# Kernel optimization log

Hardware: AMD Instinct MI355X
Metric: run time of the kernel (lower is better)

Reference implementation:

```python
import jax, jax.numpy as jnp
import numpy as np

BLOCK = 8           # block_size
FREQ_REMOVE = 2     # freq_remove_num


def _ceil16(n: int) -> int:
    # replicate DCT.padding: four rounds of ceil-div-2, then *16
    for _ in range(4):
        n = (n + 1) // 2
    return 16 * n


def _dct_mat(N: int) -> jnp.ndarray:
    # orthonormal DCT-II matrix D s.t. (D @ v) == scipy.fftpack.dct(v, norm='ortho')
    n = jnp.arange(N, dtype=jnp.float32)
    k = n[:, None]
    D = jnp.cos(jnp.pi * (2.0 * n[None, :] + 1.0) * k / (2.0 * N))
    scale = jnp.where(jnp.arange(N) == 0, jnp.sqrt(1.0 / N), jnp.sqrt(2.0 / N)).astype(jnp.float32)
    return D * scale[:, None]


def setup_inputs() -> dict:
    key = jax.random.key(0)
    x = jax.random.uniform(key, (1, 4096, 4096), dtype=jnp.float32)  # image in [0,1)
    return {"x": x}


def reference(x) -> jnp.ndarray:
    _, h, w = x.shape
    H, W = _ceil16(h), _ceil16(w)
    h1 = (H - h) // 2
    w1 = (W - w) // 2
    x = jnp.pad(x, ((0, 0), (h1, H - h - h1), (w1, W - w - w1)))
    # (x*255).byte(): truncation; inputs in [0,1) -> floor, no uint8 wrap
    x = jnp.floor(x * 255.0)
    Hb, Wb = H // BLOCK, W // BLOCK
    # [1,H,W] -> [Hb, Wb, b, b] (drop leading singleton like iterating .numpy())
    blk = x.reshape(Hb, BLOCK, Wb, BLOCK).transpose(0, 2, 1, 3)
    # Faithful to source: dct along axis=1 (Wb block-index axis) then axis=2 (block row axis)
    Dw = _dct_mat(Wb)      # [Wb, Wb]
    Db = _dct_mat(BLOCK)   # [b, b]
    y = jnp.einsum('kw,hwij->hkij', Dw, blk)   # DCT over block-column index
    y = jnp.einsum('mi,hkij->hkmj', Db, y)     # DCT over intra-block rows
    # retain_high_freq: zero first FREQ_REMOVE rows and cols of each bxb block
    mask = jnp.ones((BLOCK, BLOCK), y.dtype).at[:FREQ_REMOVE, :].set(0.0).at[:, :FREQ_REMOVE].set(0.0)
    y = y * mask  # broadcast over [Hb, Wb, b, b]
    # permute back and flatten to [1, H, W]
    out = y.transpose(0, 2, 1, 3).reshape(1, H, W)
    return out
```

## Files before the change

### kernel.cpp

```cpp
#include <hip/hip_runtime.h>
#include <math.h>

#define ZSLAB 98304
#define DSLAB 16384
#define SBUF  13312
#define OB_PITCH 392

typedef __attribute__((ext_vector_type(8))) __bf16 bf16x8;
typedef __attribute__((ext_vector_type(4))) float  f32x4;

__device__ __forceinline__ unsigned short f2bf(float f) {
  union { float f; unsigned u; } v; v.f = f;
  unsigned r = v.u + 0x7fffu + ((v.u >> 16) & 1u);
  return (unsigned short)(r >> 16);
}
__device__ __forceinline__ float bf2f_lo(unsigned u) {
  union { unsigned u; float f; } v; v.u = u << 16; return v.f;
}
__device__ __forceinline__ float bf2f_hi(unsigned u) {
  union { unsigned u; float f; } v; v.u = u & 0xffff0000u; return v.f;
}

__device__ const float DBC[8][8] = {
  { 0.35355339f,  0.35355339f,  0.35355339f,  0.35355339f,  0.35355339f,  0.35355339f,  0.35355339f,  0.35355339f},
  { 0.49039264f,  0.41573481f,  0.27778512f,  0.09754516f, -0.09754516f, -0.27778512f, -0.41573481f, -0.49039264f},
  { 0.46193977f,  0.19134172f, -0.19134172f, -0.46193977f, -0.46193977f, -0.19134172f,  0.19134172f,  0.46193977f},
  { 0.41573481f, -0.09754516f, -0.49039264f, -0.27778512f,  0.27778512f,  0.49039264f,  0.09754516f, -0.41573481f},
  { 0.35355339f, -0.35355339f, -0.35355339f,  0.35355339f,  0.35355339f, -0.35355339f, -0.35355339f,  0.35355339f},
  { 0.27778512f, -0.49039264f,  0.09754516f,  0.41573481f, -0.41573481f, -0.09754516f,  0.49039264f, -0.27778512f},
  { 0.19134172f, -0.46193977f,  0.46193977f, -0.19134172f, -0.19134172f,  0.46193977f, -0.46193977f,  0.19134172f},
  { 0.09754516f, -0.27778512f,  0.41573481f, -0.49039264f,  0.49039264f, -0.41573481f,  0.27778512f, -0.09754516f}
};

__global__ __launch_bounds__(256) void pack_all(const float* __restrict__ x,
                                                unsigned short* __restrict__ zc,
                                                unsigned short* __restrict__ dwf) {
  const int h = blockIdx.x, t = threadIdx.x;

  {
    const int idx = (blockIdx.y * 512 + blockIdx.x) * 256 + t;
    const int k = idx >> 9, w = idx & 511;
    const int n = (k * (2 * w + 1)) & 2047;
    const float c = __cosf((float)n * 0.0030679615757712823f);
    const float scale = (k == 0) ? 0.04419417382415922f : 0.0625f;
    const int kko = w >> 5, g = (w >> 3) & 3, e = w & 7, s = (k >> 1) & 3;
    dwf[(size_t)kko * DSLAB + k * 32 + ((g ^ s) << 3) + e] = f2bf(c * scale);
  }

  const int c0 = blockIdx.y * 2048 + t * 8;
  const float* xb = x + (size_t)(h * 8) * 4096 + c0;
  float q[8][8];
#pragma unroll
  for (int i = 0; i < 8; ++i) {
    float4 a = *reinterpret_cast<const float4*>(xb + (size_t)i * 4096);
    float4 b = *reinterpret_cast<const float4*>(xb + (size_t)i * 4096 + 4);
    q[i][0] = floorf(a.x * 255.0f); q[i][1] = floorf(a.y * 255.0f);
    q[i][2] = floorf(a.z * 255.0f); q[i][3] = floorf(a.w * 255.0f);
    q[i][4] = floorf(b.x * 255.0f); q[i][5] = floorf(b.y * 255.0f);
    q[i][6] = floorf(b.z * 255.0f); q[i][7] = floorf(b.w * 255.0f);
  }
  const int w0 = c0 >> 3;
  const int kko = w0 >> 5, g = (w0 >> 3) & 3, e = w0 & 7;
#pragma unroll
  for (int m = 2; m < 8; ++m) {
    const int row = h * 6 + (m - 2);
    const int s = (row >> 1) & 3;
    const size_t base = (size_t)row * 32 + ((g ^ s) << 3) + e;
#pragma unroll
    for (int j = 2; j < 8; ++j) {
      float v = 0.0f;
#pragma unroll
      for (int i = 0; i < 8; ++i) v = fmaf(DBC[m][i], q[i][j], v);
      zc[(size_t)((j - 2) * 16 + kko) * ZSLAB + base] = f2bf(v);
    }
  }
}

__device__ __forceinline__ void gload16(const unsigned short* g, unsigned short* l) {
  __builtin_amdgcn_global_load_lds(
      (__attribute__((address_space(1))) void*)(g),
      (__attribute__((address_space(3))) void*)(l),
      16, 0, 0);
}

__global__ __launch_bounds__(768, 3) void fused_dct(const unsigned short* __restrict__ zc,
                                                    const unsigned short* __restrict__ dwf,
                                                    float* __restrict__ out) {
  const int bid = blockIdx.x;
  const int mt  = bid & 63;
  const int np  = bid >> 6;

  __shared__ __align__(16) unsigned char SM[106496];
  unsigned short* SMu  = (unsigned short*)SM;
  unsigned short* Obuf = (unsigned short*)SM;

  const int tid  = threadIdx.x;
  const int lane = tid & 63;
  const int wv   = tid >> 6;
  const int j2   = wv >> 1;
  const int nh   = wv & 1;
  const int l15  = lane & 15;
  const int hi   = lane >> 4;

  const unsigned short *sA0, *sA1, *sB0, *sB1, *sB2, *sB3;
  int dA0, dA1, dB0, dB1, dB2, dB3;
  {
    const int f0 = tid, f1 = 576 + tid;
    sA0 = zc + (size_t)(f0 / 192) * 16 * ZSLAB + mt * 1536 + (f0 % 192) * 8;
    sA1 = zc + (size_t)(f1 / 192) * 16 * ZSLAB + mt * 1536 + (f1 % 192) * 8;
    dA0 = f0 * 8; dA1 = f1 * 8;
    const int bt = tid - 576;
    const int g0 = bt, g1 = 128 + bt, g2 = 256 + bt, g3 = 384 + bt;
    sB0 = dwf + (np * 2 + 0) * 2048 + (g0 & 255) * 8;
    sB1 = dwf + (np * 2 + 0) * 2048 + (g1 & 255) * 8;
    sB2 = dwf + (np * 2 + 1) * 2048 + (g2 & 255) * 8;
    sB3 = dwf + (np * 2 + 1) * 2048 + (g3 & 255) * 8;
    dB0 = 9216 + g0 * 8; dB1 = 9216 + g1 * 8; dB2 = 9216 + g2 * 8; dB3 = 9216 + g3 * 8;
  }

#define STAGE(buf, kko)                                                       \
  do {                                                                        \
    unsigned short* L_ = SMu + (buf) * SBUF;                                  \
    if (tid < 576) {                                                          \
      gload16(sA0 + (size_t)(kko) * ZSLAB, L_ + dA0);                         \
      gload16(sA1 + (size_t)(kko) * ZSLAB, L_ + dA1);                         \
    } else if (tid < 704) {                                                   \
      gload16(sB0 + (size_t)(kko) * DSLAB, L_ + dB0);                         \
      gload16(sB1 + (size_t)(kko) * DSLAB, L_ + dB1);                         \
      gload16(sB2 + (size_t)(kko) * DSLAB, L_ + dB2);                         \
      gload16(sB3 + (size_t)(kko) * DSLAB, L_ + dB3);                         \
    }                                                                         \
  } while (0)

  float* const zbase = out + (size_t)(mt * 64) * 4096 + np * 1024;
#define WAITW(na, nb, t)                                                      \
  do {                                                                        \
    if (wv < 9) {                                                             \
      asm volatile("s_waitcnt vmcnt(" #na ")" ::: "memory");                  \
      __builtin_amdgcn_sched_barrier(0);                                      \
    } else if (wv < 11) {                                                     \
      asm volatile("s_waitcnt vmcnt(" #nb ")" ::: "memory");                  \
      __builtin_amdgcn_sched_barrier(0);                                      \
    } else {                                                                  \
      _Pragma("unroll")                                                       \
      for (int q_ = 0; q_ < 4; ++q_) {                                        \
        const int e_ = (t) * 4 + q_;                                          \
        const int r16_ = e_ >> 2;                                             \
        float* p_ = zbase + (size_t)((r16_ >> 1) * 8 + (r16_ & 1)) * 4096 +   \
                    (e_ & 3) * 256 + lane * 4;                                \
        *reinterpret_cast<f32x4*>(p_) = (f32x4){0.f, 0.f, 0.f, 0.f};          \
      }                                                                       \
    }                                                                         \
  } while (0)

  int aoff[3], boffA[2], boffB[2];
#pragma unroll
  for (int mf = 0; mf < 3; ++mf) {
    const int r_ = mf * 16 + l15;
    aoff[mf] = j2 * 1536 + r_ * 32 + ((hi ^ ((r_ >> 1) & 3)) << 3);
  }
#pragma unroll
  for (int nf = 0; nf < 2; ++nf) {
    const int r_ = nh * 32 + nf * 16 + l15;
    const int sw = r_ * 32 + ((hi ^ ((r_ >> 1) & 3)) << 3);
    boffA[nf] = 9216 + sw;
    boffB[nf] = 11264 + sw;
  }

  f32x4 accA[3][2] = {}, accB[3][2] = {};

  STAGE(0, 0); STAGE(1, 1); STAGE(2, 2); STAGE(3, 3);
#pragma unroll
  for (int t = 0; t < 16; ++t) {
    if (t <= 12)      WAITW(6, 12, t);
    else if (t == 13) WAITW(4, 8, t);
    else if (t == 14) WAITW(2, 4, t);
    else              WAITW(0, 0, t);
    __builtin_amdgcn_s_barrier();
    {
      const unsigned short* Bb = SMu + (t & 3) * SBUF;
      bf16x8 afr[3], bfa[2], bfb[2];
#pragma unroll
      for (int mf = 0; mf < 3; ++mf)
        afr[mf] = *reinterpret_cast<const bf16x8*>(Bb + aoff[mf]);
#pragma unroll
      for (int nf = 0; nf < 2; ++nf) {
        bfa[nf] = *reinterpret_cast<const bf16x8*>(Bb + boffA[nf]);
        bfb[nf] = *reinterpret_cast<const bf16x8*>(Bb + boffB[nf]);
      }
      __builtin_amdgcn_s_setprio(1);
#pragma unroll
      for (int mf = 0; mf < 3; ++mf) {
        accA[mf][0] = __builtin_amdgcn_mfma_f32_16x16x32_bf16(afr[mf], bfa[0], accA[mf][0], 0, 0, 0);
        accA[mf][1] = __builtin_amdgcn_mfma_f32_16x16x32_bf16(afr[mf], bfa[1], accA[mf][1], 0, 0, 0);
        accB[mf][0] = __builtin_amdgcn_mfma_f32_16x16x32_bf16(afr[mf], bfb[0], accB[mf][0], 0, 0, 0);
        accB[mf][1] = __builtin_amdgcn_mfma_f32_16x16x32_bf16(afr[mf], bfb[1], accB[mf][1], 0, 0, 0);
      }
      __builtin_amdgcn_s_setprio(0);
    }
    asm volatile("s_waitcnt lgkmcnt(0)" ::: "memory");
    __builtin_amdgcn_s_barrier();
    if (t <= 11) STAGE(t & 3, t + 4);
  }
#undef STAGE
#undef WAITW

  __syncthreads();

#pragma unroll
  for (int tt = 0; tt < 2; ++tt) {
#pragma unroll
    for (int mf = 0; mf < 3; ++mf)
#pragma unroll
      for (int nf = 0; nf < 2; ++nf)
#pragma unroll
        for (int p = 0; p < 4; ++p) {
          const float vv = tt ? accB[mf][nf][p] : accA[mf][nf][p];
          Obuf[(mf * 16 + hi * 4 + p) * OB_PITCH + (nh * 32 + nf * 16 + l15) * 6 + j2] =
              f2bf(vv);
        }
    asm volatile("s_waitcnt lgkmcnt(0)" ::: "memory");
    __builtin_amdgcn_s_barrier();

    float* outt = out + (size_t)(mt * 64) * 4096 + (np * 2 + tt) * 512;
    for (int v = tid; v < 6144; v += 768) {
      const int row48 = v >> 7;
      const int c4 = (v & 127) << 2;
      const int hg = row48 / 6, mm = row48 - hg * 6;
      const int row64 = hg * 8 + 2 + mm;
      const int kk = c4 >> 3, jb = c4 & 4;
      const unsigned short* Ob = Obuf + row48 * OB_PITCH + kk * 6;
      const unsigned ua = *(const unsigned*)(Ob + (jb >> 1));
      const unsigned ub = *(const unsigned*)(Ob + 4);
      f32x4 val;
      if (jb) {
        val[0] = bf2f_lo(ua); val[1] = bf2f_hi(ua);
        val[2] = bf2f_lo(ub); val[3] = bf2f_hi(ub);
      } else {
        val[0] = 0.f; val[1] = 0.f;
        val[2] = bf2f_lo(ua); val[3] = bf2f_hi(ua);
      }
      *reinterpret_cast<f32x4*>(outt + (size_t)row64 * 4096 + c4) = val;
    }
    if (tt == 0) {
      asm volatile("s_waitcnt lgkmcnt(0)" ::: "memory");
      __builtin_amdgcn_s_barrier();
    }
  }
}

extern "C" void kernel_launch(void* const* d_in, const int* in_sizes, int n_in,
                              void* d_out, int out_size, void* d_ws, size_t ws_size,
                              hipStream_t stream) {
  const float* x = (const float*)d_in[0];
  float* out = (float*)d_out;
  char* ws = (char*)d_ws;

  unsigned short* dwf = (unsigned short*)ws;
  unsigned short* zc  = (unsigned short*)(ws + 524288);

  pack_all<<<dim3(512, 2), 256, 0, stream>>>(x, zc, dwf);
  fused_dct<<<256, 768, 0, stream>>>(zc, dwf, out);
}
```

Before: 41.88 us.

## Double K-step per stage with two larger LDS buffers and single-pass epilogue

The K loop now processes two K sub-slices per pipeline stage (8 iterations instead of 16), using two double-sized LDS buffers instead of four smaller ones. Each stage issues twice as many global-to-LDS loads and twice as many zero-fill stores. The epilogue writes both output halves to LDS at once and stores them in one pass, which removes a barrier round. This cuts barriers and waitcnt stalls, but pipeline prefetch depth drops from 3 stages ahead to 1, which risks exposing load latency.

```diff
diff --git a/kernel.cpp b/kernel.cpp
--- a/kernel.cpp
+++ b/kernel.cpp
@@ -3,8 +3,8 @@
 
 #define ZSLAB 98304
 #define DSLAB 16384
-#define SBUF  13312
-#define OB_PITCH 392
+#define SBUF  26624
+#define OB_PITCH 776
 
 typedef __attribute__((ext_vector_type(8))) __bf16 bf16x8;
 typedef __attribute__((ext_vector_type(4))) float  f32x4;
@@ -102,33 +102,36 @@
   const int l15  = lane & 15;
   const int hi   = lane >> 4;
 
-  const unsigned short *sA0, *sA1, *sB0, *sB1, *sB2, *sB3;
-  int dA0, dA1, dB0, dB1, dB2, dB3;
-  {
-    const int f0 = tid, f1 = 576 + tid;
-    sA0 = zc + (size_t)(f0 / 192) * 16 * ZSLAB + mt * 1536 + (f0 % 192) * 8;
-    sA1 = zc + (size_t)(f1 / 192) * 16 * ZSLAB + mt * 1536 + (f1 % 192) * 8;
-    dA0 = f0 * 8; dA1 = f1 * 8;
-    const int bt = tid - 576;
-    const int g0 = bt, g1 = 128 + bt, g2 = 256 + bt, g3 = 384 + bt;
-    sB0 = dwf + (np * 2 + 0) * 2048 + (g0 & 255) * 8;
-    sB1 = dwf + (np * 2 + 0) * 2048 + (g1 & 255) * 8;
-    sB2 = dwf + (np * 2 + 1) * 2048 + (g2 & 255) * 8;
-    sB3 = dwf + (np * 2 + 1) * 2048 + (g3 & 255) * 8;
-    dB0 = 9216 + g0 * 8; dB1 = 9216 + g1 * 8; dB2 = 9216 + g2 * 8; dB3 = 9216 + g3 * 8;
-  }
-
-#define STAGE(buf, kko)                                                       \
+  const unsigned short *sA[4], *sB[8];
+  int dA[4], dB[8];
+  if (tid < 576) {
+#pragma unroll
+    for (int q = 0; q < 4; ++q) {
+      const int f = q * 576 + tid;
+      sA[q] = zc + (size_t)((f / 384) * 16 + (f % 384) / 192) * ZSLAB + mt * 1536 +
+              (f % 192) * 8;
+      dA[q] = f * 8;
+    }
+  } else if (tid < 704) {
+#pragma unroll
+    for (int q = 0; q < 8; ++q) {
+      const int g = q * 128 + (tid - 576);
+      sB[q] = dwf + (size_t)(g >> 9) * DSLAB + np * 4096 + (g & 511) * 8;
+      dB[q] = 18432 + g * 8;
+    }
+  }
+
+#define STAGE(buf, kk)                                                        \
   do {                                                                        \
     unsigned short* L_ = SMu + (buf) * SBUF;                                  \
     if (tid < 576) {                                                          \
-      gload16(sA0 + (size_t)(kko) * ZSLAB, L_ + dA0);                         \
-      gload16(sA1 + (size_t)(kko) * ZSLAB, L_ + dA1);                         \
+      _Pragma("unroll")                                                       \
+      for (int q_ = 0; q_ < 4; ++q_)                                          \
+        gload16(sA[q_] + (size_t)(2 * (kk)) * ZSLAB, L_ + dA[q_]);            \
     } else if (tid < 704) {                                                   \
-      gload16(sB0 + (size_t)(kko) * DSLAB, L_ + dB0);                         \
-      gload16(sB1 + (size_t)(kko) * DSLAB, L_ + dB1);                         \
-      gload16(sB2 + (size_t)(kko) * DSLAB, L_ + dB2);                         \
-      gload16(sB3 + (size_t)(kko) * DSLAB, L_ + dB3);                         \
+      _Pragma("unroll")                                                       \
+      for (int q_ = 0; q_ < 8; ++q_)                                          \
+        gload16(sB[q_] + (size_t)(2 * (kk)) * DSLAB, L_ + dB[q_]);            \
     }                                                                         \
   } while (0)
 
@@ -143,9 +146,9 @@
       __builtin_amdgcn_sched_barrier(0);                                      \
     } else {                                                                  \
       _Pragma("unroll")                                                       \
-      for (int q_ = 0; q_ < 4; ++q_) {                                        \
-        const int e_ = (t) * 4 + q_;                                          \
-        const int r16_ = e_ >> 2;                                             \
+      for (int q_ = 0; q_ < 8; ++q_) {                                        \
+        const int e_ = (t) * 8 + q_;                               \
+        const int r16_ = e_ >> 2;                         \
         float* p_ = zbase + (size_t)((r16_ >> 1) * 8 + (r16_ & 1)) * 4096 +   \
                     (e_ & 3) * 256 + lane * 4;                                \
         *reinterpret_cast<f32x4*>(p_) = (f32x4){0.f, 0.f, 0.f, 0.f};          \
@@ -153,62 +156,63 @@
     }                                                                         \
   } while (0)
 
-  int aoff[3], boffA[2], boffB[2];
-#pragma unroll
-  for (int mf = 0; mf < 3; ++mf) {
-    const int r_ = mf * 16 + l15;
-    aoff[mf] = j2 * 1536 + r_ * 32 + ((hi ^ ((r_ >> 1) & 3)) << 3);
-  }
-#pragma unroll
-  for (int nf = 0; nf < 2; ++nf) {
-    const int r_ = nh * 32 + nf * 16 + l15;
-    const int sw = r_ * 32 + ((hi ^ ((r_ >> 1) & 3)) << 3);
-    boffA[nf] = 9216 + sw;
-    boffB[nf] = 11264 + sw;
+  int aoff[2][3], boff[2][2][2];
+#pragma unroll
+  for (int ks = 0; ks < 2; ++ks) {
+#pragma unroll
+    for (int mf = 0; mf < 3; ++mf) {
+      const int r_ = mf * 16 + l15;
+      aoff[ks][mf] = (j2 * 2 + ks) * 1536 + r_ * 32 + ((hi ^ ((r_ >> 1) & 3)) << 3);
+    }
+#pragma unroll
+    for (int tt = 0; tt < 2; ++tt)
+#pragma unroll
+      for (int nf = 0; nf < 2; ++nf) {
+        const int k_ = tt * 64 + nh * 32 + nf * 16 + l15;
+        boff[ks][tt][nf] = 18432 + ks * 4096 + k_ * 32 + ((hi ^ ((k_ >> 1) & 3)) << 3);
+      }
   }
 
   f32x4 accA[3][2] = {}, accB[3][2] = {};
 
-  STAGE(0, 0); STAGE(1, 1); STAGE(2, 2); STAGE(3, 3);
-#pragma unroll
-  for (int t = 0; t < 16; ++t) {
-    if (t <= 12)      WAITW(6, 12, t);
-    else if (t == 13) WAITW(4, 8, t);
-    else if (t == 14) WAITW(2, 4, t);
-    else              WAITW(0, 0, t);
+  STAGE(0, 0); STAGE(1, 1);
+#pragma unroll
+  for (int t = 0; t < 8; ++t) {
+    if (t <= 6) WAITW(4, 8, t); else WAITW(0, 0, t);
     __builtin_amdgcn_s_barrier();
     {
-      const unsigned short* Bb = SMu + (t & 3) * SBUF;
-      bf16x8 afr[3], bfa[2], bfb[2];
-#pragma unroll
-      for (int mf = 0; mf < 3; ++mf)
-        afr[mf] = *reinterpret_cast<const bf16x8*>(Bb + aoff[mf]);
-#pragma unroll
-      for (int nf = 0; nf < 2; ++nf) {
-        bfa[nf] = *reinterpret_cast<const bf16x8*>(Bb + boffA[nf]);
-        bfb[nf] = *reinterpret_cast<const bf16x8*>(Bb + boffB[nf]);
+      const unsigned short* Bb = SMu + (t & 1) * SBUF;
+#pragma unroll
+      for (int ks = 0; ks < 2; ++ks) {
+        bf16x8 afr[3], bfa[2], bfb[2];
+#pragma unroll
+        for (int mf = 0; mf < 3; ++mf)
+          afr[mf] = *reinterpret_cast<const bf16x8*>(Bb + aoff[ks][mf]);
+#pragma unroll
+        for (int nf = 0; nf < 2; ++nf) {
+          bfa[nf] = *reinterpret_cast<const bf16x8*>(Bb + boff[ks][0][nf]);
+          bfb[nf] = *reinterpret_cast<const bf16x8*>(Bb + boff[ks][1][nf]);
+        }
+        __builtin_amdgcn_s_setprio(1);
+#pragma unroll
+        for (int mf = 0; mf < 3; ++mf) {
+          accA[mf][0] = __builtin_amdgcn_mfma_f32_16x16x32_bf16(afr[mf], bfa[0], accA[mf][0], 0, 0, 0);
+          accA[mf][1] = __builtin_amdgcn_mfma_f32_16x16x32_bf16(afr[mf], bfa[1], accA[mf][1], 0, 0, 0);
+          accB[mf][0] = __builtin_amdgcn_mfma_f32_16x16x32_bf16(afr[mf], bfb[0], accB[mf][0], 0, 0, 0);
+          accB[mf][1] = __builtin_amdgcn_mfma_f32_16x16x32_bf16(afr[mf], bfb[1], accB[mf][1], 0, 0, 0);
+        }
+        __builtin_amdgcn_s_setprio(0);
       }
-      __builtin_amdgcn_s_setprio(1);
-#pragma unroll
-      for (int mf = 0; mf < 3; ++mf) {
-        accA[mf][0] = __builtin_amdgcn_mfma_f32_16x16x32_bf16(afr[mf], bfa[0], accA[mf][0], 0, 0, 0);
-        accA[mf][1] = __builtin_amdgcn_mfma_f32_16x16x32_bf16(afr[mf], bfa[1], accA[mf][1], 0, 0, 0);
-        accB[mf][0] = __builtin_amdgcn_mfma_f32_16x16x32_bf16(afr[mf], bfb[0], accB[mf][0], 0, 0, 0);
-        accB[mf][1] = __builtin_amdgcn_mfma_f32_16x16x32_bf16(afr[mf], bfb[1], accB[mf][1], 0, 0, 0);
-      }
-      __builtin_amdgcn_s_setprio(0);
     }
     asm volatile("s_waitcnt lgkmcnt(0)" ::: "memory");
     __builtin_amdgcn_s_barrier();
-    if (t <= 11) STAGE(t & 3, t + 4);
+    if (t <= 5) STAGE(t & 1, t + 2);
   }
 #undef STAGE
 #undef WAITW
 
-  __syncthreads();
-
-#pragma unroll
-  for (int tt = 0; tt < 2; ++tt) {
+#pragma unroll
+  for (int tt = 0; tt < 2; ++tt)
 #pragma unroll
     for (int mf = 0; mf < 3; ++mf)
 #pragma unroll
@@ -216,36 +220,31 @@
 #pragma unroll
         for (int p = 0; p < 4; ++p) {
           const float vv = tt ? accB[mf][nf][p] : accA[mf][nf][p];
-          Obuf[(mf * 16 + hi * 4 + p) * OB_PITCH + (nh * 32 + nf * 16 + l15) * 6 + j2] =
-              f2bf(vv);
+          Obuf[(mf * 16 + hi * 4 + p) * OB_PITCH +
+               (tt * 64 + nh * 32 + nf * 16 + l15) * 6 + j2] = f2bf(vv);
         }
-    asm volatile("s_waitcnt lgkmcnt(0)" ::: "memory");
-    __builtin_amdgcn_s_barrier();
-
-    float* outt = out + (size_t)(mt * 64) * 4096 + (np * 2 + tt) * 512;
-    for (int v = tid; v < 6144; v += 768) {
-      const int row48 = v >> 7;
-      const int c4 = (v & 127) << 2;
-      const int hg = row48 / 6, mm = row48 - hg * 6;
-      const int row64 = hg * 8 + 2 + mm;
-      const int kk = c4 >> 3, jb = c4 & 4;
-      const unsigned short* Ob = Obuf + row48 * OB_PITCH + kk * 6;
-      const unsigned ua = *(const unsigned*)(Ob + (jb >> 1));
-      const unsigned ub = *(const unsigned*)(Ob + 4);
-      f32x4 val;
-      if (jb) {
-        val[0] = bf2f_lo(ua); val[1] = bf2f_hi(ua);
-        val[2] = bf2f_lo(ub); val[3] = bf2f_hi(ub);
-      } else {
-        val[0] = 0.f; val[1] = 0.f;
-        val[2] = bf2f_lo(ua); val[3] = bf2f_hi(ua);
-      }
-      *reinterpret_cast<f32x4*>(outt + (size_t)row64 * 4096 + c4) = val;
-    }
-    if (tt == 0) {
-      asm volatile("s_waitcnt lgkmcnt(0)" ::: "memory");
-      __builtin_amdgcn_s_barrier();
-    }
+  asm volatile("s_waitcnt lgkmcnt(0)" ::: "memory");
+  __builtin_amdgcn_s_barrier();
+
+  float* outt = out + (size_t)(mt * 64) * 4096 + np * 1024;
+  for (int v = tid; v < 12288; v += 768) {
+    const int row48 = v >> 8;
+    const int c4 = (v & 255) << 2;
+    const int hg = row48 / 6, mm = row48 - hg * 6;
+    const int row64 = hg * 8 + 2 + mm;
+    const int kk = c4 >> 3, jb = c4 & 4;
+    const unsigned short* Ob = Obuf + row48 * OB_PITCH + kk * 6;
+    const unsigned ua = *(const unsigned*)(Ob + (jb >> 1));
+    const unsigned ub = *(const unsigned*)(Ob + 4);
+    f32x4 val;
+    if (jb) {
+      val[0] = bf2f_lo(ua); val[1] = bf2f_hi(ua);
+      val[2] = bf2f_lo(ub); val[3] = bf2f_hi(ub);
+    } else {
+      val[0] = 0.f; val[1] = 0.f;
+      val[2] = bf2f_lo(ua); val[3] = bf2f_hi(ua);
+    }
+    *reinterpret_cast<f32x4*>(outt + (size_t)row64 * 4096 + c4) = val;
   }
 }
 
```

Measured after the change: 43.54 us. +4.0%, slower.
